# Kernel optimization log

Measured on AMD Instinct MI355X. Metric: run time of the kernel, lower is better.

The kernel has to match this reference:

```python
import jax, jax.numpy as jnp
import numpy as np

N, D, H = 4096, 512, 8
HD = D // H
KEEP_RATIO = 0.5
EPS = 1e-6

def setup_inputs() -> dict:
    key = jax.random.key(0)
    ks = jax.random.split(key, 10)
    s = 1.0 / np.sqrt(D)
    return {
        'stock_feats': jax.random.normal(ks[0], (N, D), jnp.float32),
        'z_primary': jax.random.normal(ks[1], (1, D), jnp.float32),
        'z_secondary': jax.random.normal(ks[2], (1, D), jnp.float32),
        'Wq': jax.random.normal(ks[3], (D, D), jnp.float32) * s,
        'Wk': jax.random.normal(ks[4], (D, D), jnp.float32) * s,
        'Wv': jax.random.normal(ks[5], (D, D), jnp.float32) * s,
        'Wg': jax.random.normal(ks[6], (D, 2 * D), jnp.float32) * s,
        'bg': jnp.zeros((D,), jnp.float32),
        'Wag': jax.random.normal(ks[7], (D, 2 * D), jnp.float32) * s,
        'bag': jnp.zeros((D,), jnp.float32),
        'norm_w': jnp.ones((D,), jnp.float32),
        'Wo': jax.random.normal(ks[8], (D, D), jnp.float32) * s,
        'bo': jnp.zeros((D,), jnp.float32),
    }

def reference(stock_feats, z_primary, z_secondary, Wq, Wk, Wv, Wg, bg, Wag, bag, norm_w, Wo, bo):
    scale = 1.0 / np.sqrt(HD)
    nodes = jnp.concatenate([z_primary, z_secondary, stock_feats], axis=0)  # [N+2, D]
    # regime-gated queries
    z_concat = jnp.concatenate([z_primary, z_secondary], axis=-1)  # [1, 2D]
    regime_mod = jax.nn.sigmoid(z_concat @ Wg.T + bg)              # [1, D]
    q = ((stock_feats @ Wq.T) * regime_mod).reshape(N, H, HD)
    k = (nodes @ Wk.T).reshape(N + 2, H, HD)
    v = (nodes @ Wv.T).reshape(N + 2, H, HD)
    scores = jnp.einsum('nhd,mhd->nhm', q, k) * scale              # [N, H, N+2]
    raw_scores = scores.mean(axis=1)                               # [N, N+2]
    # top-k mask over stock (non-anchor) columns
    anchor_scores = scores[..., :2]
    stock_scores = scores[..., 2:]                                 # [N, H, N]
    k_keep = max(5, int(N * KEEP_RATIO))
    topk_val = jax.lax.top_k(stock_scores, k_keep)[0]
    threshold = topk_val[..., -1:]
    stock_scores = jnp.where(stock_scores >= threshold, stock_scores, -1e9)
    scores_m = jnp.concatenate([anchor_scores, stock_scores], axis=-1)
    attn = jax.nn.softmax(scores_m, axis=-1)                       # [N, H, N+2]
    out = jnp.einsum('nhm,mhd->nhd', attn, v).reshape(N, D)
    out = out @ Wo.T + bo
    # alpha guard: gated residual + RMSNorm
    gate = jax.nn.sigmoid(jnp.concatenate([stock_feats, out], axis=-1) @ Wag.T + bag)
    gr = stock_feats + gate * out
    rms = jax.lax.rsqrt(jnp.mean(gr * gr, axis=-1, keepdims=True) + EPS)
    final_out = gr * rms * norm_w
    return (final_out, raw_scores, gate.mean(), attn.mean(axis=1))
```

## Files before the change

kernel.cpp:

```cpp
#include <hip/hip_runtime.h>
#include <hip/hip_fp16.h>
#include <math.h>

#define NS 4096
#define DIM 512
#define NH 8
#define HD 64
#define M2 4098
#define MPAD 4224
#define KKEEP 2048u

#define OUT_F 0
#define OUT_R 2097152
#define OUT_G 18882560
#define OUT_A 18882561

typedef __attribute__((ext_vector_type(8))) short bf16x8;
typedef __attribute__((ext_vector_type(4))) float f32x4;

__device__ __forceinline__ float sigmoidf_(float x) { return 1.0f / (1.0f + __expf(-x)); }

__device__ __forceinline__ unsigned short btrunc(float f) {
  unsigned u = __float_as_uint(f);
  u = u + 0x7FFFu + ((u >> 16) & 1u);
  return (unsigned short)(u >> 16);
}
__device__ __forceinline__ float bton(unsigned short h) {
  return __uint_as_float(((unsigned)h) << 16);
}

__device__ __forceinline__ void scan_pick(unsigned c0, unsigned c1, unsigned c2, unsigned c3,
                                          unsigned k_rem, int lane,
                                          unsigned& bsel_out, unsigned& nxt_out) {
  unsigned run = c0 + c1 + c2 + c3;
  #pragma unroll
  for (int off = 1; off < 64; off <<= 1) {
    unsigned o_ = __shfl_down(run, off, 64);
    if (lane + off < 64) run += o_;
  }
  unsigned s0 = run, s1 = run - c0, s2 = s1 - c1, s3 = s2 - c2, s4 = s3 - c3;
  int which = -1;
  if      (s0 >= k_rem && s1 < k_rem) which = 0;
  else if (s1 >= k_rem && s2 < k_rem) which = 1;
  else if (s2 >= k_rem && s3 < k_rem) which = 2;
  else if (s3 >= k_rem && s4 < k_rem) which = 3;
  unsigned long long bal = __ballot(which >= 0);
  int src = (int)__ffsll(bal) - 1;
  unsigned nxtv = (which == 0) ? s1 : (which == 1) ? s2 : (which == 2) ? s3 : s4;
  unsigned bsel = (unsigned)(4 * lane + (which < 0 ? 0 : which));
  bsel_out = (unsigned)__shfl((int)bsel, src, 64);
  nxt_out  = (unsigned)__shfl((int)nxtv, src, 64);
}

__global__ __launch_bounds__(256) void regime_kernel(
    const float* __restrict__ zp, const float* __restrict__ zs,
    const float* __restrict__ Wg, const float* __restrict__ bg,
    float* __restrict__ regime) {
  __shared__ float zc[1024];
  int t = threadIdx.x;
  for (int i = t; i < 512; i += 256) { zc[i] = zp[i]; zc[512 + i] = zs[i]; }
  __syncthreads();
  for (int j = t; j < 512; j += 256) {
    const float4* w = (const float4*)(Wg + (size_t)j * 1024);
    float acc = 0.f;
    #pragma unroll 8
    for (int i = 0; i < 256; i++) {
      float4 wv = w[i];
      acc += wv.x * zc[4*i] + wv.y * zc[4*i+1] + wv.z * zc[4*i+2] + wv.w * zc[4*i+3];
    }
    regime[j] = sigmoidf_(acc + bg[j]);
  }
}

__global__ __launch_bounds__(256) void conv_bf(
    const float* __restrict__ src, unsigned short* __restrict__ dst, int n4) {
  int i4 = blockIdx.x * 256 + threadIdx.x;
  if (i4 >= n4) return;
  float4 v = *(const float4*)(src + (size_t)i4 * 4);
  ushort4 o; o.x = btrunc(v.x); o.y = btrunc(v.y); o.z = btrunc(v.z); o.w = btrunc(v.w);
  *(ushort4*)(dst + (size_t)i4 * 4) = o;
}

__global__ __launch_bounds__(256) void build_nodes_bf(
    const float* __restrict__ zp, const float* __restrict__ zs,
    const float* __restrict__ sf, unsigned short* __restrict__ nb) {
  int i4 = blockIdx.x * 256 + threadIdx.x;
  if (i4 >= (M2 * DIM) / 4) return;
  int idx = i4 * 4;
  int m = idx >> 9, c = idx & 511;
  const float* src = (m == 0) ? (zp + c) : (m == 1) ? (zs + c)
                               : (sf + (size_t)(m - 2) * 512 + c);
  float4 v = *(const float4*)src;
  ushort4 o; o.x = btrunc(v.x); o.y = btrunc(v.y); o.z = btrunc(v.z); o.w = btrunc(v.w);
  *(ushort4*)(nb + idx) = o;
}

#define LSTR 40
__global__ __launch_bounds__(256) void gemm_bf16(
    const unsigned short* __restrict__ A, const unsigned short* __restrict__ B,
    const float* __restrict__ bias, const float* __restrict__ cscale,
    const float* __restrict__ rscale,
    float* __restrict__ Cf, unsigned short* __restrict__ Cb,
    int M, int N, int K, int lda, int ldb, int ldc, float scale, int mode,
    size_t sA, size_t sB, size_t sC, size_t sR, int kz, int ksz) {
  __shared__ unsigned short As[128 * LSTR];
  __shared__ unsigned short Bs[128 * LSTR];
  const int z = blockIdx.z;
  const int zh = z / kz, zc = z - zh * kz;
  A += (size_t)zh * sA + (size_t)zc * ksz;
  B += (size_t)zh * sB + (size_t)zc * ksz;
  if (Cf) Cf += (size_t)zh * sC;
  if (Cb) Cb += (size_t)zh * sC;
  if (rscale) rscale += (size_t)zh * sR;
  const int t = threadIdx.x;
  const int w = t >> 6, lane = t & 63;
  const int wr = w >> 1, wc = w & 1;
  const int lr = lane & 15, lg = lane >> 4;
  const int bm = blockIdx.y * 128, bn = blockIdx.x * 128;
  f32x4 acc[4][4] = {};
  for (int k0 = 0; k0 < K; k0 += 32) {
    #pragma unroll
    for (int i = 0; i < 2; i++) {
      int q = t + i * 256;
      int row = q >> 2;
      int ko = (q & 3) * 8;
      bf16x8 av = {};
      int gr = bm + row;
      if (gr < M) av = *(const bf16x8*)(A + (size_t)gr * lda + k0 + ko);
      *(bf16x8*)(As + row * LSTR + ko) = av;
      bf16x8 bv = {};
      int gbr = bn + row;
      if (gbr < N) bv = *(const bf16x8*)(B + (size_t)gbr * ldb + k0 + ko);
      *(bf16x8*)(Bs + row * LSTR + ko) = bv;
    }
    __syncthreads();
    {
      bf16x8 af[4], bfr[4];
      #pragma unroll
      for (int i = 0; i < 4; i++)
        af[i] = *(const bf16x8*)(As + (64 * wr + 16 * i + lr) * LSTR + lg * 8);
      #pragma unroll
      for (int j = 0; j < 4; j++)
        bfr[j] = *(const bf16x8*)(Bs + (64 * wc + 16 * j + lr) * LSTR + lg * 8);
      #pragma unroll
      for (int i = 0; i < 4; i++)
        #pragma unroll
        for (int j = 0; j < 4; j++)
          acc[i][j] = __builtin_amdgcn_mfma_f32_16x16x32_bf16(af[i], bfr[j], acc[i][j], 0, 0, 0);
    }
    __syncthreads();
  }
  #pragma unroll
  for (int i = 0; i < 4; i++) {
    #pragma unroll
    for (int j = 0; j < 4; j++) {
      #pragma unroll
      for (int q = 0; q < 4; q++) {
        int row = bm + 64 * wr + 16 * i + lg * 4 + q;
        int col = bn + 64 * wc + 16 * j + lr;
        if (row < M && col < N) {
          float v = acc[i][j][q] * scale;
          if (bias)   v += bias[col];
          if (cscale) v *= cscale[col];
          if (rscale) v *= rscale[row];
          if (mode == 0)      Cf[(size_t)row * ldc + col] = v;
          else if (mode == 1) Cb[(size_t)row * ldc + col] = btrunc(v);
          else if (mode == 2) Cb[(size_t)col * ldc + row] = btrunc(v);
          else                atomicAdd(&Cf[(size_t)row * ldc + col], v);
        }
      }
    }
  }
}

__global__ __launch_bounds__(256) void gemm_n64(
    const unsigned short* __restrict__ A, const unsigned short* __restrict__ B,
    const float* __restrict__ bias, const float* __restrict__ cscale,
    const float* __restrict__ rscale,
    float* __restrict__ Cf, unsigned short* __restrict__ Cb,
    int M, int N, int K, int lda, int ldb, int ldc, float scale, int mode,
    size_t sA, size_t sB, size_t sC, size_t sR, int kz, int ksz) {
  __shared__ unsigned short As[128 * LSTR];
  __shared__ unsigned short Bs[64 * LSTR];
  const int z = blockIdx.z;
  const int zh = z / kz, zc = z - zh * kz;
  A += (size_t)zh * sA + (size_t)zc * ksz;
  B += (size_t)zh * sB + (size_t)zc * ksz;
  if (Cf) Cf += (size_t)zh * sC;
  if (Cb) Cb += (size_t)zh * sC;
  if (rscale) rscale += (size_t)zh * sR;
  const int t = threadIdx.x;
  const int w = t >> 6, lane = t & 63;
  const int lr = lane & 15, lg = lane >> 4;
  const int bm = blockIdx.y * 128, bn = blockIdx.x * 64;
  f32x4 acc[2][4] = {};
  for (int k0 = 0; k0 < K; k0 += 32) {
    {
      #pragma unroll
      for (int i = 0; i < 2; i++) {
        int q = t + i * 256;
        int row = q >> 2;
        int ko = (q & 3) * 8;
        bf16x8 av = {};
        int gr = bm + row;
        if (gr < M) av = *(const bf16x8*)(A + (size_t)gr * lda + k0 + ko);
        *(bf16x8*)(As + row * LSTR + ko) = av;
      }
      int row = t >> 2;
      int ko = (t & 3) * 8;
      bf16x8 bv = {};
      int gbr = bn + row;
      if (gbr < N) bv = *(const bf16x8*)(B + (size_t)gbr * ldb + k0 + ko);
      *(bf16x8*)(Bs + row * LSTR + ko) = bv;
    }
    __syncthreads();
    {
      bf16x8 af[2], bfr[4];
      #pragma unroll
      for (int i = 0; i < 2; i++)
        af[i] = *(const bf16x8*)(As + (32 * w + 16 * i + lr) * LSTR + lg * 8);
      #pragma unroll
      for (int j = 0; j < 4; j++)
        bfr[j] = *(const bf16x8*)(Bs + (16 * j + lr) * LSTR + lg * 8);
      #pragma unroll
      for (int i = 0; i < 2; i++)
        #pragma unroll
        for (int j = 0; j < 4; j++)
          acc[i][j] = __builtin_amdgcn_mfma_f32_16x16x32_bf16(af[i], bfr[j], acc[i][j], 0, 0, 0);
    }
    __syncthreads();
  }
  #pragma unroll
  for (int i = 0; i < 2; i++) {
    #pragma unroll
    for (int j = 0; j < 4; j++) {
      #pragma unroll
      for (int q = 0; q < 4; q++) {
        int row = bm + 32 * w + 16 * i + lg * 4 + q;
        int col = bn + 16 * j + lr;
        if (row < M && col < N) {
          float v = acc[i][j][q] * scale;
          if (bias)   v += bias[col];
          if (cscale) v *= cscale[col];
          if (rscale) v *= rscale[row];
          if (mode == 0)      Cf[(size_t)row * ldc + col] = v;
          else if (mode == 1) Cb[(size_t)row * ldc + col] = btrunc(v);
          else if (mode == 2) Cb[(size_t)col * ldc + row] = btrunc(v);
          else                atomicAdd(&Cf[(size_t)row * ldc + col], v);
        }
      }
    }
  }
}

#define SSMEM (8 * MPAD * 2 + 8 * 256 * 4 + 32)
__global__ __launch_bounds__(512) void select_softmax(
    unsigned short* __restrict__ S, float* __restrict__ Zg, float* __restrict__ outA) {
  extern __shared__ char sm[];
  unsigned short* keys = (unsigned short*)sm;
  unsigned* hist = (unsigned*)(sm + 8 * MPAD * 2);
  float* Zs = (float*)(sm + 8 * MPAD * 2 + 8 * 256 * 4);
  const int w = threadIdx.x >> 6, lane = threadIdx.x & 63;
  const int n = blockIdx.x;
  const size_t row = (size_t)w * 4096 + n;
  unsigned short* kr = keys + w * MPAD;
  unsigned* hw = hist + w * 256;
  unsigned short* g = S + row * MPAD;
  unsigned a0k = 0, a1k = 0;

  hw[lane] = 0u; hw[lane + 64] = 0u; hw[lane + 128] = 0u; hw[lane + 192] = 0u;
  unsigned maxkey = 0;
  #pragma unroll
  for (int c = 0; c < 9; ++c) {
    if (c < 8 || lane < 16) {
      uint4 v = *(const uint4*)(g + c * 512 + lane * 8);
      unsigned* pv = (unsigned*)&v;
      int mb = c * 512 + lane * 8;
      #pragma unroll
      for (int p2 = 0; p2 < 4; ++p2) {
        unsigned pk = pv[p2], outw = 0;
        #pragma unroll
        for (int e = 0; e < 2; ++e) {
          int m = mb + 2 * p2 + e;
          unsigned u = (e == 0) ? (pk & 0xFFFFu) : (pk >> 16);
          unsigned key = u ^ ((u & 0x8000u) ? 0xFFFFu : 0x8000u);
          if (m < 2) { if (m == 0) a0k = key; else a1k = key; key = 0u; }
          else if (m >= M2) key = 0u;
          outw |= key << (16 * e);
          atomicAdd(&hw[key >> 8], 1u);
          if (key > maxkey) maxkey = key;
        }
        *(unsigned*)(kr + mb + 2 * p2) = outw;
      }
    }
  }
  if (a0k > maxkey) maxkey = a0k;
  if (a1k > maxkey) maxkey = a1k;
  #pragma unroll
  for (int off = 32; off > 0; off >>= 1) {
    unsigned o_ = (unsigned)__shfl_xor((int)maxkey, off, 64);
    if (o_ > maxkey) maxkey = o_;
  }
  float lmax = bton((unsigned short)(maxkey ^ ((maxkey & 0x8000u) ? 0x8000u : 0xFFFFu)));

  unsigned tb, k_rem = KKEEP;
  {
    unsigned c0 = hw[4*lane], c1 = hw[4*lane+1], c2 = hw[4*lane+2], c3 = hw[4*lane+3];
    unsigned nxtv;
    scan_pick(c0, c1, c2, c3, k_rem, lane, tb, nxtv);
    k_rem -= nxtv;
  }

  hw[lane] = 0u; hw[lane + 64] = 0u; hw[lane + 128] = 0u; hw[lane + 192] = 0u;
  #pragma unroll
  for (int c = 0; c < 9; ++c) {
    if (c < 8 || lane < 16) {
      uint4 v = *(const uint4*)(kr + c * 512 + lane * 8);
      const unsigned* pv = (const unsigned*)&v;
      #pragma unroll
      for (int p2 = 0; p2 < 4; ++p2) {
        unsigned lo = pv[p2] & 0xFFFFu, hi = pv[p2] >> 16;
        if ((lo >> 8) == tb) atomicAdd(&hw[lo & 255u], 1u);
        if ((hi >> 8) == tb) atomicAdd(&hw[hi & 255u], 1u);
      }
    }
  }
  unsigned thrkey;
  {
    unsigned c0 = hw[4*lane], c1 = hw[4*lane+1], c2 = hw[4*lane+2], c3 = hw[4*lane+3];
    unsigned bsel, nxtv;
    scan_pick(c0, c1, c2, c3, k_rem, lane, bsel, nxtv);
    thrkey = (tb << 8) | bsel;
  }

  float lsum = 0.f;
  #pragma unroll
  for (int c = 0; c < 9; ++c) {
    if (c < 8 || lane < 16) {
      uint4 v = *(const uint4*)(kr + c * 512 + lane * 8);
      unsigned* pv = (unsigned*)&v;
      #pragma unroll
      for (int p2 = 0; p2 < 4; ++p2) {
        unsigned pk = pv[p2], outw = 0;
        bool anc = (c == 0 && lane == 0 && p2 == 0);
        if (anc) pk = a0k | (a1k << 16);
        #pragma unroll
        for (int e = 0; e < 2; ++e) {
          unsigned key = (e == 0) ? (pk & 0xFFFFu) : (pk >> 16);
          bool kept = anc || (key >= thrkey);
          unsigned short us = (unsigned short)(key ^ ((key & 0x8000u) ? 0x8000u : 0xFFFFu));
          float ev = kept ? __expf(bton(us) - lmax) : 0.f;
          unsigned short eb = btrunc(ev);
          lsum += bton(eb);
          outw |= ((unsigned)eb) << (16 * e);
        }
        pv[p2] = outw;
      }
      *(uint4*)(kr + c * 512 + lane * 8) = v;
      *(uint4*)(g + c * 512 + lane * 8) = v;
    }
  }
  #pragma unroll
  for (int off = 32; off > 0; off >>= 1) lsum += __shfl_xor(lsum, off, 64);
  float invZ = 1.0f / lsum;
  if (lane == 0) { Zg[row] = invZ; Zs[w] = invZ; }
  __syncthreads();

  for (int m = threadIdx.x; m < M2; m += 512) {
    float s = 0.f;
    #pragma unroll
    for (int h = 0; h < 8; ++h)
      s += bton(keys[h * MPAD + m]) * Zs[h];
    outA[(size_t)n * M2 + m] = s * 0.125f;
  }
}

#define SROWB 8464
#define QOFF  (16 * SROWB)
#define HOFF  (QOFF + 16 * 72 * 2)
#define AOFF  (HOFF + 16 * 256 * 4)
#define SMEMSZ (AOFF + 64)

__global__ __launch_bounds__(1024) void fused_attn(
    const unsigned short* __restrict__ Qbf, const unsigned short* __restrict__ Kbf,
    const unsigned short* __restrict__ Vt, unsigned short* __restrict__ aobf,
    float* __restrict__ attn_mean_out) {
  extern __shared__ char dsm[];
  unsigned short* qt = (unsigned short*)(dsm + QOFF);
  unsigned* hist = (unsigned*)(dsm + HOFF);
  unsigned short* anchk = (unsigned short*)(dsm + AOFF);
  const int n0 = blockIdx.x * 16;
  const int t = threadIdx.x;
  const int w = t >> 6, lane = t & 63;
  const int lr = lane & 15, lg = lane >> 4;
  unsigned* hw = hist + w * 256;
  const int r = w;
  const unsigned swz = (unsigned)((r & 7) << 4);

  for (int h = 0; h < NH; ++h) {
    qt[(t >> 6) * 72 + (t & 63)] = Qbf[(size_t)(n0 + (t >> 6)) * DIM + h * HD + (t & 63)];
    __syncthreads();
    {
      bf16x8 a0 = *(const bf16x8*)(qt + lr * 72 + lg * 8);
      bf16x8 a1 = *(const bf16x8*)(qt + lr * 72 + 32 + lg * 8);
      #pragma unroll
      for (int f = 0; f < 17; ++f) {
        if (f < 16 || w < 8) {
          int m0 = (w + 16 * f) * 16;
          const unsigned short* kp = Kbf + (size_t)(m0 + lr) * DIM + h * HD + lg * 8;
          bf16x8 b0 = *(const bf16x8*)(kp);
          bf16x8 b1 = *(const bf16x8*)(kp + 32);
          f32x4 c = {0.f, 0.f, 0.f, 0.f};
          c = __builtin_amdgcn_mfma_f32_16x16x32_bf16(a0, b0, c, 0, 0, 0);
          c = __builtin_amdgcn_mfma_f32_16x16x32_bf16(a1, b1, c, 0, 0, 0);
          int m = m0 + lr;
          #pragma unroll
          for (int q = 0; q < 4; ++q) {
            int rr = lg * 4 + q;
            unsigned short us = btrunc(c[q] * 0.125f);
            unsigned key = (unsigned)us ^ ((us & 0x8000u) ? 0xFFFFu : 0x8000u);
            unsigned short stor = (m >= M2 || m < 2) ? (unsigned short)0 : (unsigned short)key;
            *(unsigned short*)(dsm + rr * SROWB + ((2 * m) ^ ((rr & 7) << 4))) = stor;
            if (m < 2) anchk[rr * 2 + m] = (unsigned short)key;
          }
        }
      }
    }
    __syncthreads();

    float invZ;
    {
      unsigned maxkey = 0;
      hw[lane] = 0u; hw[lane + 64] = 0u; hw[lane + 128] = 0u; hw[lane + 192] = 0u;
      #pragma unroll
      for (int c = 0; c < 9; ++c) {
        if (c < 8 || lane < 16) {
          uint4 pk4 = *(const uint4*)(dsm + r * SROWB + (((unsigned)(c * 1024 + lane * 16)) ^ swz));
          const unsigned* pw = (const unsigned*)&pk4;
          #pragma unroll
          for (int p2 = 0; p2 < 4; ++p2) {
            unsigned pk = pw[p2];
            unsigned lo = pk & 0xFFFFu, hi = pk >> 16;
            atomicAdd(&hw[lo >> 8], 1u);
            atomicAdd(&hw[hi >> 8], 1u);
            if (lo > maxkey) maxkey = lo;
            if (hi > maxkey) maxkey = hi;
          }
        }
      }
      #pragma unroll
      for (int off = 32; off > 0; off >>= 1) {
        unsigned o_ = (unsigned)__shfl_xor((int)maxkey, off, 64);
        if (o_ > maxkey) maxkey = o_;
      }
      {
        unsigned a0 = anchk[2 * r], a1 = anchk[2 * r + 1];
        if (a0 > maxkey) maxkey = a0;
        if (a1 > maxkey) maxkey = a1;
      }
      float lmax = bton((unsigned short)(maxkey ^ ((maxkey & 0x8000u) ? 0x8000u : 0xFFFFu)));

      unsigned tb, k_rem = KKEEP;
      {
        unsigned c0 = hw[4*lane], c1 = hw[4*lane+1], c2 = hw[4*lane+2], c3 = hw[4*lane+3];
        unsigned nxtv;
        scan_pick(c0, c1, c2, c3, k_rem, lane, tb, nxtv);
        k_rem -= nxtv;
      }
      hw[lane] = 0u; hw[lane + 64] = 0u; hw[lane + 128] = 0u; hw[lane + 192] = 0u;
      #pragma unroll
      for (int c = 0; c < 9; ++c) {
        if (c < 8 || lane < 16) {
          uint4 pk4 = *(const uint4*)(dsm + r * SROWB + (((unsigned)(c * 1024 + lane * 16)) ^ swz));
          const unsigned* pw = (const unsigned*)&pk4;
          #pragma unroll
          for (int p2 = 0; p2 < 4; ++p2) {
            unsigned pk = pw[p2];
            unsigned lo = pk & 0xFFFFu, hi = pk >> 16;
            if ((lo >> 8) == tb) atomicAdd(&hw[lo & 255u], 1u);
            if ((hi >> 8) == tb) atomicAdd(&hw[hi & 255u], 1u);
          }
        }
      }
      unsigned thrkey;
      {
        unsigned c0 = hw[4*lane], c1 = hw[4*lane+1], c2 = hw[4*lane+2], c3 = hw[4*lane+3];
        unsigned bsel, nxtv;
        scan_pick(c0, c1, c2, c3, k_rem, lane, bsel, nxtv);
        thrkey = (tb << 8) | bsel;
      }

      float lsum = 0.f;
      #pragma unroll
      for (int c = 0; c < 9; ++c) {
        if (c < 8 || lane < 16) {
          char* ap = dsm + r * SROWB + (((unsigned)(c * 1024 + lane * 16)) ^ swz);
          uint4 pk4 = *(const uint4*)ap;
          unsigned* pw = (unsigned*)&pk4;
          #pragma unroll
          for (int p2 = 0; p2 < 4; ++p2) {
            unsigned pk = pw[p2];
            bool anc = (c == 0 && lane == 0 && p2 == 0);
            if (anc) pk = (unsigned)anchk[2 * r] | ((unsigned)anchk[2 * r + 1] << 16);
            unsigned outw = 0;
            #pragma unroll
            for (int e = 0; e < 2; ++e) {
              unsigned key = (e == 0) ? (pk & 0xFFFFu) : (pk >> 16);
              bool kept = anc || (key >= thrkey);
              unsigned short us = (unsigned short)(key ^ ((key & 0x8000u) ? 0x8000u : 0xFFFFu));
              float evf = kept ? __expf(bton(us) - lmax) : 0.f;
              unsigned short eb = btrunc(evf);
              lsum += bton(eb);
              outw |= ((unsigned)eb) << (16 * e);
            }
            pw[p2] = outw;
          }
          *(uint4*)ap = pk4;
        }
      }
      #pragma unroll
      for (int off = 32; off > 0; off >>= 1) lsum += __shfl_xor(lsum, off, 64);
      invZ = 1.0f / lsum;
      for (int c = 0; c < 9; ++c) {
        if (c < 8 || lane < 16) {
          const char* ap = dsm + r * SROWB + (((unsigned)(c * 1024 + lane * 16)) ^ swz);
          uint4 e4 = *(const uint4*)ap;
          const unsigned* pw = (const unsigned*)&e4;
          int bm = c * 512 + lane * 8;
          float* base = attn_mean_out + (size_t)(n0 + r) * M2 + bm;
          #pragma unroll
          for (int p2 = 0; p2 < 4; ++p2) {
            float v0 = bton((unsigned short)(pw[p2] & 0xFFFFu)) * invZ * 0.125f;
            float v1 = bton((unsigned short)(pw[p2] >> 16)) * invZ * 0.125f;
            int m = bm + 2 * p2;
            if (m < M2)     { if (h == 0) base[2*p2] = v0;   else base[2*p2] += v0; }
            if (m + 1 < M2) { if (h == 0) base[2*p2+1] = v1; else base[2*p2+1] += v1; }
          }
        }
      }
    }
    __syncthreads();

    {
      f32x4 o0 = {0.f,0.f,0.f,0.f}, o1 = o0, o2 = o0, o3 = o0;
      const unsigned short* Vb = Vt + (size_t)(h * HD) * MPAD;
      #pragma unroll
      for (int ks = 0; ks < 9; ++ks) {
        if (ks < 8 || w < 4) {
          int kk = (w + 16 * ks) * 32 + lg * 8;
          bf16x8 a = *(const bf16x8*)(dsm + lr * SROWB + ((2 * kk) ^ ((lr & 7) << 4)));
          {
            bf16x8 b0 = *(const bf16x8*)(Vb + (size_t)(lr) * MPAD + kk);
            bf16x8 b1 = *(const bf16x8*)(Vb + (size_t)(16 + lr) * MPAD + kk);
            o0 = __builtin_amdgcn_mfma_f32_16x16x32_bf16(a, b0, o0, 0, 0, 0);
            o1 = __builtin_amdgcn_mfma_f32_16x16x32_bf16(a, b1, o1, 0, 0, 0);
          }
          {
            bf16x8 b2 = *(const bf16x8*)(Vb + (size_t)(32 + lr) * MPAD + kk);
            bf16x8 b3 = *(const bf16x8*)(Vb + (size_t)(48 + lr) * MPAD + kk);
            o2 = __builtin_amdgcn_mfma_f32_16x16x32_bf16(a, b2, o2, 0, 0, 0);
            o3 = __builtin_amdgcn_mfma_f32_16x16x32_bf16(a, b3, o3, 0, 0, 0);
          }
        }
      }
      __syncthreads();
      float* part = (float*)dsm;
      #pragma unroll
      for (int q = 0; q < 4; q++) {
        int row = lg * 4 + q;
        part[w * 1024 + row * 64 +      lr] = o0[q];
        part[w * 1024 + row * 64 + 16 + lr] = o1[q];
        part[w * 1024 + row * 64 + 32 + lr] = o2[q];
        part[w * 1024 + row * 64 + 48 + lr] = o3[q];
      }
      __syncthreads();
      {
        float s = 0.f;
        #pragma unroll
        for (int ww = 0; ww < 16; ++ww) s += part[ww * 1024 + t];
        aobf[(size_t)(n0 + (t >> 6)) * DIM + h * HD + (t & 63)] = btrunc(s * invZ);
      }
    }
  }
}

__global__ __launch_bounds__(256) void cat_bf(
    const unsigned short* __restrict__ sfbf, const float* __restrict__ pj,
    unsigned short* __restrict__ cat) {
  int i4 = blockIdx.x * 256 + threadIdx.x;
  if (i4 >= (4096 * 1024) / 4) return;
  int idx = i4 * 4;
  int n = idx >> 10, c = idx & 1023;
  if (c < 512) {
    *(ushort4*)(cat + idx) = *(const ushort4*)(sfbf + (size_t)n * 512 + c);
  } else {
    float4 v = *(const float4*)(pj + (size_t)n * 512 + (c - 512));
    ushort4 o; o.x = btrunc(v.x); o.y = btrunc(v.y); o.z = btrunc(v.z); o.w = btrunc(v.w);
    *(ushort4*)(cat + idx) = o;
  }
}

__global__ __launch_bounds__(256) void final_kernel(
    const float* __restrict__ sf, const float* __restrict__ pj,
    const float* __restrict__ gl, const float* __restrict__ norm_w,
    float* __restrict__ outf, float* __restrict__ gpart) {
  int n = blockIdx.x, t = threadIdx.x;
  __shared__ float red[256];
  size_t base = (size_t)n * 512;
  float g0 = sigmoidf_(gl[base + t]);
  float g1 = sigmoidf_(gl[base + 256 + t]);
  float x0 = sf[base + t], x1 = sf[base + 256 + t];
  float p0 = pj[base + t], p1 = pj[base + 256 + t];
  float gr0 = x0 + g0 * p0, gr1 = x1 + g1 * p1;

  red[t] = g0 + g1;
  __syncthreads();
  for (int off = 128; off > 0; off >>= 1) {
    if (t < off) red[t] += red[t + off];
    __syncthreads();
  }
  if (t == 0) gpart[n] = red[0];
  __syncthreads();

  red[t] = gr0 * gr0 + gr1 * gr1;
  __syncthreads();
  for (int off = 128; off > 0; off >>= 1) {
    if (t < off) red[t] += red[t + off];
    __syncthreads();
  }
  float rms = rsqrtf(red[0] * (1.0f / 512.0f) + 1e-6f);
  outf[base + t] = gr0 * rms * norm_w[t];
  outf[base + 256 + t] = gr1 * rms * norm_w[256 + t];
}

__global__ __launch_bounds__(256) void gate_reduce(
    const float* __restrict__ gpart, float* __restrict__ out_scalar) {
  __shared__ float red[256];
  int t = threadIdx.x;
  float s = 0.f;
  for (int i = t; i < 4096; i += 256) s += gpart[i];
  red[t] = s;
  __syncthreads();
  for (int off = 128; off > 0; off >>= 1) {
    if (t < off) red[t] += red[t + off];
    __syncthreads();
  }
  if (t == 0) out_scalar[0] = red[0] * (1.0f / (4096.0f * 512.0f));
}

extern "C" void kernel_launch(void* const* d_in, const int* in_sizes, int n_in,
                              void* d_out, int out_size, void* d_ws, size_t ws_size,
                              hipStream_t stream) {
  const float* sf  = (const float*)d_in[0];
  const float* zp  = (const float*)d_in[1];
  const float* zs  = (const float*)d_in[2];
  const float* Wq  = (const float*)d_in[3];
  const float* Wk  = (const float*)d_in[4];
  const float* Wv  = (const float*)d_in[5];
  const float* Wg  = (const float*)d_in[6];
  const float* bg  = (const float*)d_in[7];
  const float* Wag = (const float*)d_in[8];
  const float* bag = (const float*)d_in[9];
  const float* nw  = (const float*)d_in[10];
  const float* Wo  = (const float*)d_in[11];
  const float* bo  = (const float*)d_in[12];

  float* out  = (float*)d_out;
  float* outF = out + OUT_F;
  float* outR = out + OUT_R;
  float* outG = out + OUT_G;
  float* outA = out + OUT_A;

  char* W = (char*)d_ws;
  float*          regime  = (float*)(W + 0);
  float*          gpart   = (float*)(W + 2048);
  unsigned short* sfbf    = (unsigned short*)(W + 18432);
  unsigned short* nodesbf = (unsigned short*)(W + 4212736);
  unsigned short* Qbf     = (unsigned short*)(W + 8409088);
  unsigned short* Kbf     = (unsigned short*)(W + 12603392);
  unsigned short* Vt      = (unsigned short*)(W + 16928768);
  unsigned short* aobf    = (unsigned short*)(W + 21254144);
  unsigned short* catbf   = (unsigned short*)(W + 25448448);
  unsigned short* Wqbf    = (unsigned short*)(W + 33837056);
  unsigned short* Wkbf    = (unsigned short*)(W + 34361344);
  unsigned short* Wvbf    = (unsigned short*)(W + 34885632);
  unsigned short* Wobf    = (unsigned short*)(W + 35409920);
  unsigned short* Wagbf   = (unsigned short*)(W + 35934208);
  float*          pj      = (float*)(W + 36982784);
  float*          gl      = (float*)(W + 4212736);
  unsigned short* Splane  = (unsigned short*)(W + 45371392);
  float*          Zg      = (float*)(W + 322195456);
  float*          aopf    = (float*)(W + 322326528);
  const size_t need_s = 330715136ull;
  const int use_s = (ws_size >= need_s) ? 1 : 0;

  hipFuncSetAttribute((const void*)fused_attn,
                      hipFuncAttributeMaxDynamicSharedMemorySize, SMEMSZ);
  hipFuncSetAttribute((const void*)select_softmax,
                      hipFuncAttributeMaxDynamicSharedMemorySize, SSMEM);

  regime_kernel<<<1, 256, 0, stream>>>(zp, zs, Wg, bg, regime);
  conv_bf<<<2048, 256, 0, stream>>>(sf, sfbf, 524288);
  build_nodes_bf<<<2049, 256, 0, stream>>>(zp, zs, sf, nodesbf);
  conv_bf<<<256, 256, 0, stream>>>(Wq, Wqbf, 65536);
  conv_bf<<<256, 256, 0, stream>>>(Wk, Wkbf, 65536);
  conv_bf<<<256, 256, 0, stream>>>(Wv, Wvbf, 65536);
  conv_bf<<<256, 256, 0, stream>>>(Wo, Wobf, 65536);
  conv_bf<<<512, 256, 0, stream>>>(Wag, Wagbf, 131072);
  hipMemsetAsync(Kbf, 0, 4325376, stream);
  hipMemsetAsync(Vt, 0, 4325376, stream);

  gemm_n64<<<dim3(8, 32, 1), 256, 0, stream>>>(sfbf, Wqbf, nullptr, regime, nullptr, nullptr, Qbf,
                                               4096, 512, 512, 512, 512, 512, 1.0f, 1, 0, 0, 0, 0, 1, 0);
  gemm_n64<<<dim3(8, 33, 1), 256, 0, stream>>>(nodesbf, Wkbf, nullptr, nullptr, nullptr, nullptr, Kbf,
                                               M2, 512, 512, 512, 512, 512, 1.0f, 1, 0, 0, 0, 0, 1, 0);
  gemm_n64<<<dim3(8, 33, 1), 256, 0, stream>>>(nodesbf, Wvbf, nullptr, nullptr, nullptr, nullptr, Vt,
                                               M2, 512, 512, 512, 512, MPAD, 1.0f, 2, 0, 0, 0, 0, 1, 0);

  gemm_bf16<<<dim3(33, 32, 1), 256, 0, stream>>>(Qbf, Kbf, nullptr, nullptr, nullptr, outR, nullptr,
                                                 4096, M2, 512, 512, 512, M2, 0.015625f, 0, 0, 0, 0, 0, 1, 0);

  if (use_s) {
    gemm_bf16<<<dim3(33, 32, 8), 256, 0, stream>>>(Qbf, Kbf, nullptr, nullptr, nullptr, nullptr, Splane,
                                                   4096, M2, 64, 512, 512, MPAD, 0.125f, 1,
                                                   64, 64, (size_t)4096 * MPAD, 0, 1, 0);
    select_softmax<<<4096, 512, SSMEM, stream>>>(Splane, Zg, outA);
    hipMemsetAsync(aopf, 0, 8388608, stream);
    gemm_n64<<<dim3(1, 32, 16), 256, 0, stream>>>(Splane, Vt, nullptr, nullptr, Zg, aopf, nullptr,
                                                  4096, 64, 2112, MPAD, MPAD, 512, 1.0f, 3,
                                                  (size_t)4096 * MPAD, (size_t)64 * MPAD, 64, 4096, 2, 2112);
    conv_bf<<<2048, 256, 0, stream>>>(aopf, aobf, 524288);
  } else {
    fused_attn<<<256, 1024, SMEMSZ, stream>>>(Qbf, Kbf, Vt, aobf, outA);
  }

  gemm_n64<<<dim3(8, 32, 1), 256, 0, stream>>>(aobf, Wobf, bo, nullptr, nullptr, pj, nullptr,
                                               4096, 512, 512, 512, 512, 512, 1.0f, 0, 0, 0, 0, 0, 1, 0);
  cat_bf<<<4096, 256, 0, stream>>>(sfbf, pj, catbf);
  gemm_n64<<<dim3(8, 32, 1), 256, 0, stream>>>(catbf, Wagbf, bag, nullptr, nullptr, gl, nullptr,
                                               4096, 512, 1024, 1024, 1024, 512, 1.0f, 0, 0, 0, 0, 0, 1, 0);
  final_kernel<<<4096, 256, 0, stream>>>(sf, pj, gl, nw, outF, gpart);
  gate_reduce<<<1, 256, 0, stream>>>(gpart, outG);
}
```

Measured before the change: 814.6 us.

## Fold raw-score mean into select_softmax and privatize histograms across lane copies

On the use_s path, the separate full-K QK^T GEMM that produced raw_scores is dropped. Raw scores are now computed inside select_softmax by averaging the eight per-head score planes that are already stored. The kernel also stops staging keys in shared memory and re-reads the global score row on each pass, which frees LDS. It spends that space on four histogram copies per wave to reduce atomic contention. The cost is extra global re-reads and precision: raw_scores now comes from bf16 per-head scores rather than an fp32 GEMM output.

```diff
diff --git a/kernel.cpp b/kernel.cpp
--- a/kernel.cpp
+++ b/kernel.cpp
@@ -253,32 +253,33 @@
   }
 }
 
-#define SSMEM (8 * MPAD * 2 + 8 * 256 * 4 + 32)
+#define HCPY 264
+#define SSMEM (8 * 4 * HCPY * 4 + 64)
 __global__ __launch_bounds__(512) void select_softmax(
-    unsigned short* __restrict__ S, float* __restrict__ Zg, float* __restrict__ outA) {
+    unsigned short* __restrict__ S, float* __restrict__ Zg,
+    float* __restrict__ outA, float* __restrict__ outR) {
   extern __shared__ char sm[];
-  unsigned short* keys = (unsigned short*)sm;
-  unsigned* hist = (unsigned*)(sm + 8 * MPAD * 2);
-  float* Zs = (float*)(sm + 8 * MPAD * 2 + 8 * 256 * 4);
+  unsigned* hist = (unsigned*)sm;
+  float* Zs = (float*)(sm + 8 * 4 * HCPY * 4);
   const int w = threadIdx.x >> 6, lane = threadIdx.x & 63;
   const int n = blockIdx.x;
   const size_t row = (size_t)w * 4096 + n;
-  unsigned short* kr = keys + w * MPAD;
-  unsigned* hw = hist + w * 256;
+  unsigned* hw = hist + w * (4 * HCPY);
+  unsigned* hc = hw + (lane & 3) * HCPY;
   unsigned short* g = S + row * MPAD;
   unsigned a0k = 0, a1k = 0;
 
-  hw[lane] = 0u; hw[lane + 64] = 0u; hw[lane + 128] = 0u; hw[lane + 192] = 0u;
+  for (int i = lane; i < 4 * HCPY; i += 64) hw[i] = 0u;
   unsigned maxkey = 0;
   #pragma unroll
   for (int c = 0; c < 9; ++c) {
     if (c < 8 || lane < 16) {
       uint4 v = *(const uint4*)(g + c * 512 + lane * 8);
-      unsigned* pv = (unsigned*)&v;
+      const unsigned* pv = (const unsigned*)&v;
       int mb = c * 512 + lane * 8;
       #pragma unroll
       for (int p2 = 0; p2 < 4; ++p2) {
-        unsigned pk = pv[p2], outw = 0;
+        unsigned pk = pv[p2];
         #pragma unroll
         for (int e = 0; e < 2; ++e) {
           int m = mb + 2 * p2 + e;
@@ -286,11 +287,9 @@
           unsigned key = u ^ ((u & 0x8000u) ? 0xFFFFu : 0x8000u);
           if (m < 2) { if (m == 0) a0k = key; else a1k = key; key = 0u; }
           else if (m >= M2) key = 0u;
-          outw |= key << (16 * e);
-          atomicAdd(&hw[key >> 8], 1u);
+          atomicAdd(&hc[key >> 8], 1u);
           if (key > maxkey) maxkey = key;
         }
-        *(unsigned*)(kr + mb + 2 * p2) = outw;
       }
     }
   }
@@ -305,49 +304,76 @@
 
   unsigned tb, k_rem = KKEEP;
   {
-    unsigned c0 = hw[4*lane], c1 = hw[4*lane+1], c2 = hw[4*lane+2], c3 = hw[4*lane+3];
+    unsigned c0 = hw[4*lane] + hw[HCPY+4*lane] + hw[2*HCPY+4*lane] + hw[3*HCPY+4*lane];
+    unsigned c1 = hw[4*lane+1] + hw[HCPY+4*lane+1] + hw[2*HCPY+4*lane+1] + hw[3*HCPY+4*lane+1];
+    unsigned c2 = hw[4*lane+2] + hw[HCPY+4*lane+2] + hw[2*HCPY+4*lane+2] + hw[3*HCPY+4*lane+2];
+    unsigned c3 = hw[4*lane+3] + hw[HCPY+4*lane+3] + hw[2*HCPY+4*lane+3] + hw[3*HCPY+4*lane+3];
     unsigned nxtv;
     scan_pick(c0, c1, c2, c3, k_rem, lane, tb, nxtv);
     k_rem -= nxtv;
   }
 
-  hw[lane] = 0u; hw[lane + 64] = 0u; hw[lane + 128] = 0u; hw[lane + 192] = 0u;
+  for (int i = lane; i < 4 * HCPY; i += 64) hw[i] = 0u;
   #pragma unroll
   for (int c = 0; c < 9; ++c) {
     if (c < 8 || lane < 16) {
-      uint4 v = *(const uint4*)(kr + c * 512 + lane * 8);
+      uint4 v = *(const uint4*)(g + c * 512 + lane * 8);
       const unsigned* pv = (const unsigned*)&v;
+      int mb = c * 512 + lane * 8;
       #pragma unroll
       for (int p2 = 0; p2 < 4; ++p2) {
-        unsigned lo = pv[p2] & 0xFFFFu, hi = pv[p2] >> 16;
-        if ((lo >> 8) == tb) atomicAdd(&hw[lo & 255u], 1u);
-        if ((hi >> 8) == tb) atomicAdd(&hw[hi & 255u], 1u);
+        unsigned pk = pv[p2];
+        #pragma unroll
+        for (int e = 0; e < 2; ++e) {
+          int m = mb + 2 * p2 + e;
+          unsigned u = (e == 0) ? (pk & 0xFFFFu) : (pk >> 16);
+          unsigned key = u ^ ((u & 0x8000u) ? 0xFFFFu : 0x8000u);
+          bool real = (m >= 2) && (m < M2);
+          if (real && (key >> 8) == tb) atomicAdd(&hc[key & 255u], 1u);
+        }
       }
     }
   }
   unsigned thrkey;
   {
-    unsigned c0 = hw[4*lane], c1 = hw[4*lane+1], c2 = hw[4*lane+2], c3 = hw[4*lane+3];
+    unsigned c0 = hw[4*lane] + hw[HCPY+4*lane] + hw[2*HCPY+4*lane] + hw[3*HCPY+4*lane];
+    unsigned c1 = hw[4*lane+1] + hw[HCPY+4*lane+1] + hw[2*HCPY+4*lane+1] + hw[3*HCPY+4*lane+1];
+    unsigned c2 = hw[4*lane+2] + hw[HCPY+4*lane+2] + hw[2*HCPY+4*lane+2] + hw[3*HCPY+4*lane+2];
+    unsigned c3 = hw[4*lane+3] + hw[HCPY+4*lane+3] + hw[2*HCPY+4*lane+3] + hw[3*HCPY+4*lane+3];
     unsigned bsel, nxtv;
     scan_pick(c0, c1, c2, c3, k_rem, lane, bsel, nxtv);
     thrkey = (tb << 8) | bsel;
   }
+
+  for (int m = threadIdx.x; m < M2; m += 512) {
+    float s = 0.f;
+    #pragma unroll
+    for (int h = 0; h < 8; ++h)
+      s += bton(S[((size_t)h * 4096 + n) * MPAD + m]);
+    outR[(size_t)n * M2 + m] = s * 0.125f;
+  }
+  __syncthreads();
 
   float lsum = 0.f;
   #pragma unroll
   for (int c = 0; c < 9; ++c) {
     if (c < 8 || lane < 16) {
-      uint4 v = *(const uint4*)(kr + c * 512 + lane * 8);
+      uint4 v = *(const uint4*)(g + c * 512 + lane * 8);
       unsigned* pv = (unsigned*)&v;
+      int mb = c * 512 + lane * 8;
       #pragma unroll
       for (int p2 = 0; p2 < 4; ++p2) {
         unsigned pk = pv[p2], outw = 0;
-        bool anc = (c == 0 && lane == 0 && p2 == 0);
-        if (anc) pk = a0k | (a1k << 16);
+        bool anc = (mb + 2 * p2 == 0);
         #pragma unroll
         for (int e = 0; e < 2; ++e) {
-          unsigned key = (e == 0) ? (pk & 0xFFFFu) : (pk >> 16);
-          bool kept = anc || (key >= thrkey);
+          int m = mb + 2 * p2 + e;
+          unsigned u = (e == 0) ? (pk & 0xFFFFu) : (pk >> 16);
+          unsigned key = u ^ ((u & 0x8000u) ? 0xFFFFu : 0x8000u);
+          bool kept;
+          if (anc) kept = true;
+          else if (m >= M2) kept = false;
+          else kept = (key >= thrkey);
           unsigned short us = (unsigned short)(key ^ ((key & 0x8000u) ? 0x8000u : 0xFFFFu));
           float ev = kept ? __expf(bton(us) - lmax) : 0.f;
           unsigned short eb = btrunc(ev);
@@ -356,7 +382,6 @@
         }
         pv[p2] = outw;
       }
-      *(uint4*)(kr + c * 512 + lane * 8) = v;
       *(uint4*)(g + c * 512 + lane * 8) = v;
     }
   }
@@ -370,7 +395,7 @@
     float s = 0.f;
     #pragma unroll
     for (int h = 0; h < 8; ++h)
-      s += bton(keys[h * MPAD + m]) * Zs[h];
+      s += bton(S[((size_t)h * 4096 + n) * MPAD + m]) * Zs[h];
     outA[(size_t)n * M2 + m] = s * 0.125f;
   }
 }
@@ -717,20 +742,19 @@
   gemm_n64<<<dim3(8, 33, 1), 256, 0, stream>>>(nodesbf, Wvbf, nullptr, nullptr, nullptr, nullptr, Vt,
                                                M2, 512, 512, 512, 512, MPAD, 1.0f, 2, 0, 0, 0, 0, 1, 0);
 
-  gemm_bf16<<<dim3(33, 32, 1), 256, 0, stream>>>(Qbf, Kbf, nullptr, nullptr, nullptr, outR, nullptr,
-                                                 4096, M2, 512, 512, 512, M2, 0.015625f, 0, 0, 0, 0, 0, 1, 0);
-
   if (use_s) {
     gemm_bf16<<<dim3(33, 32, 8), 256, 0, stream>>>(Qbf, Kbf, nullptr, nullptr, nullptr, nullptr, Splane,
                                                    4096, M2, 64, 512, 512, MPAD, 0.125f, 1,
                                                    64, 64, (size_t)4096 * MPAD, 0, 1, 0);
-    select_softmax<<<4096, 512, SSMEM, stream>>>(Splane, Zg, outA);
+    select_softmax<<<4096, 512, SSMEM, stream>>>(Splane, Zg, outA, outR);
     hipMemsetAsync(aopf, 0, 8388608, stream);
     gemm_n64<<<dim3(1, 32, 16), 256, 0, stream>>>(Splane, Vt, nullptr, nullptr, Zg, aopf, nullptr,
                                                   4096, 64, 2112, MPAD, MPAD, 512, 1.0f, 3,
                                                   (size_t)4096 * MPAD, (size_t)64 * MPAD, 64, 4096, 2, 2112);
     conv_bf<<<2048, 256, 0, stream>>>(aopf, aobf, 524288);
   } else {
+    gemm_bf16<<<dim3(33, 32, 1), 256, 0, stream>>>(Qbf, Kbf, nullptr, nullptr, nullptr, outR, nullptr,
+                                                   4096, M2, 512, 512, 512, M2, 0.015625f, 0, 0, 0, 0, 0, 1, 0);
     fused_attn<<<256, 1024, SMEMSZ, stream>>>(Qbf, Kbf, Vt, aobf, outA);
   }
 
```

Result: no change. 817.7 us (+0.4%).
